# Kernel tuning notes

Measured on AMD Instinct MI355X. Metric: run time of the kernel, lower is better.

Reference implementation:

```python
import jax, jax.numpy as jnp
import numpy as np

N = 50000        # nodes
E = 150000       # edges
D_IN = 42        # node_input_dim
D_H = 42         # node_hidden_dim
E_IN = 10        # edge_input_dim
E_H = 128        # edge_hidden_dim
STEPS = 6        # num_step_message_passing


def _linear_params(key, fin, fout):
    k1, k2 = jax.random.split(key)
    bound = 1.0 / np.sqrt(fin)
    W = jax.random.uniform(k1, (fin, fout), minval=-bound, maxval=bound, dtype=jnp.float32)
    b = jax.random.uniform(k2, (fout,), minval=-bound, maxval=bound, dtype=jnp.float32)
    return W, b


def setup_inputs() -> dict:
    key = jax.random.key(0)
    ks = jax.random.split(key, 9)
    n_feat = jax.random.normal(ks[0], (N, D_IN), dtype=jnp.float32)
    e_feat = jax.random.normal(ks[1], (E, E_IN), dtype=jnp.float32)
    src = jax.random.randint(ks[2], (E,), 0, N, dtype=jnp.int32)
    dst = jax.random.randint(ks[3], (E,), 0, N, dtype=jnp.int32)
    lin0_w, lin0_b = _linear_params(ks[4], D_IN, D_H)
    en1_w, en1_b = _linear_params(ks[5], E_IN, E_H)
    en2_w, en2_b = _linear_params(ks[6], E_H, D_H * D_H)
    msg_w, msg_b = _linear_params(ks[7], 2 * D_H, D_H)
    conv_bias = jnp.zeros((D_H,), dtype=jnp.float32)  # NNConv bias
    return dict(n_feat=n_feat, e_feat=e_feat, src=src, dst=dst,
                lin0_w=lin0_w, lin0_b=lin0_b,
                en1_w=en1_w, en1_b=en1_b, en2_w=en2_w, en2_b=en2_b,
                conv_bias=conv_bias, msg_w=msg_w, msg_b=msg_b)


def reference(n_feat, e_feat, src, dst, lin0_w, lin0_b, en1_w, en1_b,
              en2_w, en2_b, conv_bias, msg_w, msg_b):
    init = n_feat
    out = jax.nn.relu(n_feat @ lin0_w + lin0_b)          # [N, D_H]
    # edge network: per-edge weight matrix (constant across the 6 steps)
    h_e = jax.nn.relu(e_feat @ en1_w + en1_b)            # [E, E_H]
    W_e = (h_e @ en2_w + en2_b).reshape(E, D_H, D_H)     # [E, D_H, D_H]
    for _ in range(STEPS):
        # NNConv: gather src feats, per-edge matmul, scatter-sum to dst,
        # identity residual (in==out feats) + bias
        msg = jnp.einsum('ei,eio->eo', out[src], W_e)    # [E, D_H]
        aggr = jax.ops.segment_sum(msg, dst, num_segments=N)
        m = jax.nn.relu(aggr + out + conv_bias)          # relu(conv(...))
        out = jnp.concatenate([m, out], axis=1) @ msg_w + msg_b
    return out + init
```

## Files before the change

### kernel.cpp

```cpp
#include <hip/hip_runtime.h>

typedef unsigned short u16;
typedef unsigned int u32;

#define NN 50000
#define NE 150000
#define D 42
#define EH 128
#define DD 1764
#define STEPS 6
#define MS 48
#define SCAN_NB 196

typedef __attribute__((ext_vector_type(8))) short bf8;
typedef __attribute__((ext_vector_type(4))) float f4;

static __device__ __forceinline__ float bf2f(u16 v) {
  return __uint_as_float(((u32)v) << 16);
}
static __device__ __forceinline__ u16 f2bf(float f) {
  u32 x = __float_as_uint(f);
  return (u16)((x + 0x7fffu + ((x >> 16) & 1u)) >> 16);
}

__global__ void k_detect(const u32* __restrict__ words, int* __restrict__ flag) {
  __shared__ int cnt;
  if (threadIdx.x == 0) cnt = 0;
  __syncthreads();
  int bad = 0;
  for (int i = threadIdx.x; i < 4096; i += 256) {
    u32 w = words[i];
    float v = __uint_as_float((w & 0xffffu) << 16);
    float a = fabsf(v);
    if (!(a < 16.0f)) bad++;
  }
  if (bad) atomicAdd(&cnt, bad);
  __syncthreads();
  if (threadIdx.x == 0) flag[0] = (cnt < 100) ? 1 : 0;
}

__global__ void k_cvt(const void* __restrict__ src, float* __restrict__ dst,
                      int count, const int* __restrict__ flag) {
  int i = blockIdx.x * blockDim.x + threadIdx.x;
  if (i >= count) return;
  if (flag[0]) dst[i] = bf2f(((const u16*)src)[i]);
  else         dst[i] = ((const float*)src)[i];
}

__global__ void k_hist(const int* __restrict__ dstI, int* __restrict__ cnt) {
  int e = blockIdx.x * blockDim.x + threadIdx.x;
  if (e < NE) atomicAdd(&cnt[dstI[e]], 1);
}

__global__ void k_scanA(const int* __restrict__ cnt, int* __restrict__ loc,
                        int* __restrict__ part) {
  __shared__ int wsum[4];
  int tid = threadIdx.x, wid = tid >> 6, lane = tid & 63;
  int i = blockIdx.x * 256 + tid;
  int v = (i < NN) ? cnt[i] : 0;
#pragma unroll
  for (int d = 1; d < 64; d <<= 1) {
    int t = __shfl_up(v, d, 64);
    if (lane >= d) v += t;
  }
  if (lane == 63) wsum[wid] = v;
  __syncthreads();
  if (tid == 0) {
    int s = 0;
#pragma unroll
    for (int w2 = 0; w2 < 4; ++w2) { int t = wsum[w2]; wsum[w2] = s; s += t; }
    part[blockIdx.x] = s;
  }
  __syncthreads();
  v += wsum[wid];
  if (i < NN) loc[i] = v;
}

__global__ void k_scanB(int* __restrict__ part) {
  __shared__ int wsum[4];
  int tid = threadIdx.x, wid = tid >> 6, lane = tid & 63;
  int v = (tid < SCAN_NB) ? part[tid] : 0;
  int orig = v;
#pragma unroll
  for (int d = 1; d < 64; d <<= 1) {
    int t = __shfl_up(v, d, 64);
    if (lane >= d) v += t;
  }
  if (lane == 63) wsum[wid] = v;
  __syncthreads();
  if (tid == 0) {
    int s = 0;
#pragma unroll
    for (int w2 = 0; w2 < 4; ++w2) { int t = wsum[w2]; wsum[w2] = s; s += t; }
  }
  __syncthreads();
  v += wsum[wid];
  if (tid < SCAN_NB) part[tid] = v - orig;
}

__global__ void k_scanC(const int* __restrict__ loc, const int* __restrict__ part,
                        int* __restrict__ rs) {
  int i = blockIdx.x * 256 + threadIdx.x;
  if (i == 0) rs[0] = 0;
  if (i < NN) rs[i + 1] = loc[i] + part[blockIdx.x];
}

__global__ void k_rank(const int* __restrict__ dstI, const int* __restrict__ srcI,
                       int* __restrict__ cursor, int* __restrict__ rank,
                       int* __restrict__ srcS) {
  int e = blockIdx.x * blockDim.x + threadIdx.x;
  if (e >= NE) return;
  int p = atomicAdd(&cursor[dstI[e]], 1);
  rank[e] = p;
  srcS[p] = srcI[e];
}

__global__ void k_lin0(const float* __restrict__ nf, const float* __restrict__ w,
                       const float* __restrict__ b, float* __restrict__ outp) {
  int gid = blockIdx.x * blockDim.x + threadIdx.x;
  int n = gid >> 6, lane = gid & 63;
  if (n >= NN) return;
  float xv = (lane < D) ? nf[(size_t)n * D + lane] : 0.f;
  if (lane < D) {
    float acc = b[lane];
    for (int i = 0; i < D; ++i)
      acc += __shfl(xv, i, 64) * w[i * D + lane];
    outp[(size_t)n * D + lane] = fmaxf(acc, 0.f);
  }
}

__global__ void k_en1(const float* __restrict__ ef, const float* __restrict__ w,
                      const float* __restrict__ b, const int* __restrict__ rank,
                      u16* __restrict__ h) {
  int gid = blockIdx.x * blockDim.x + threadIdx.x;
  int e = gid >> 7, k = gid & 127;
  if (e >= NE) return;
  float acc = b[k];
#pragma unroll
  for (int i = 0; i < 10; ++i)
    acc += ef[(size_t)e * 10 + i] * w[i * EH + k];
  h[(size_t)rank[e] * EH + k] = f2bf(fmaxf(acc, 0.f));
}

__global__ void k_packA(const float* __restrict__ w2, u16* __restrict__ Ap) {
  int idx = blockIdx.x * 256 + threadIdx.x;
  if (idx >= D * 4 * 3 * 64 * 8) return;
  int j = idx & 7;
  int t = idx >> 3;
  int l = t & 63; t >>= 6;
  int f = t % 3;  t /= 3;
  int s = t & 3;
  int i = t >> 2;
  int k = s * 32 + ((l >> 4) << 3) + j;
  int o = f * 16 + (l & 15);
  float v = (o < D) ? w2[(size_t)k * DD + i * D + o] : 0.f;
  Ap[idx] = f2bf(v);
}

__global__ void k_packB2(const float* __restrict__ e2b, u16* __restrict__ b2p) {
  int idx = blockIdx.x * 256 + threadIdx.x;
  if (idx >= 2 * 3 * 64 * 8) return;
  int j = idx & 7;
  int t = idx >> 3;
  int l = t & 63; t >>= 6;
  int f = t % 3;
  int s = t / 3;
  int k = s * 32 + ((l >> 4) << 3) + j;
  int o = f * 16 + (l & 15);
  float v = (k < D && o < D) ? e2b[k * D + o] : 0.f;
  b2p[idx] = f2bf(v);
}

__launch_bounds__(256, 3)
__global__ void k_edge_mfma(const float* __restrict__ outp, const u16* __restrict__ hbf,
                            const u16* __restrict__ Ap, const u16* __restrict__ b2p,
                            const int* __restrict__ srcS, float* __restrict__ msg) {
  __shared__ __align__(16) char smem[10752 + 26624];
  float* xT = (float*)smem;
  char*  hls = smem + 10752;
  char*  xbf = smem + 10752 + 16384;
  float* red = (float*)(smem + 10752);

  int tid = threadIdx.x;
  long et = (long)blockIdx.x * 64;
  int ne = (int)(NE - et); if (ne > 64) ne = 64;

  for (int c = tid; c < 1024; c += 256) {
    int row = c >> 4;
    int off = (c & 15) << 4;
    uint4 v = {0, 0, 0, 0};
    if (row < ne) v = *(const uint4*)(hbf + (et + row) * EH + (off >> 1));
    *(uint4*)(hls + row * 256 + (off ^ ((row & 7) << 4))) = v;
  }
  {
    int r = tid >> 2, j = tid & 3;
    const float* xr = (r < ne) ? (outp + (size_t)srcS[et + r] * D) : nullptr;
    for (int i = j; i < D; i += 4) {
      float v = xr ? xr[i] : 0.f;
      xT[i * 64 + r] = v;
      int bo = (r * 128 + i * 2) ^ ((r & 7) << 4);
      *(u16*)(xbf + bo) = f2bf(v);
    }
    for (int i = D + j; i < 64; i += 4) {
      int bo = (r * 128 + i * 2) ^ ((r & 7) << 4);
      *(u16*)(xbf + bo) = 0;
    }
  }
  __syncthreads();

  int w = tid >> 6;
  int l = tid & 63;
  int e16 = l & 15;
  int kg = l >> 4;

  bf8 hf[4];
  {
    int kb = (w * 32 + kg * 8) * 2;
    int sw = (e16 & 7) << 4;
#pragma unroll
    for (int g = 0; g < 4; ++g)
      hf[g] = *(const bf8*)(hls + (g * 16 + e16) * 256 + (kb ^ sw));
  }

  f4 macc[4][3];
#pragma unroll
  for (int g = 0; g < 4; ++g)
#pragma unroll
    for (int f = 0; f < 3; ++f)
      macc[g][f] = (f4){0.f, 0.f, 0.f, 0.f};

  const u16* apw = Ap + (size_t)w * 1536 + (size_t)l * 8;

#define LOADA(dst, ii)                                                          \
  {                                                                             \
    const u16* p_ = apw + (size_t)(ii) * 6144;                                  \
    dst[0] = *(const bf8*)(p_);                                                 \
    dst[1] = *(const bf8*)(p_ + 512);                                           \
    dst[2] = *(const bf8*)(p_ + 1024);                                          \
  }

#define COMPUTE(ii, AA)                                                         \
  {                                                                             \
    _Pragma("unroll")                                                           \
    for (int g = 0; g < 4; ++g) {                                               \
      float xs = xT[(ii) * 64 + g * 16 + e16];                                  \
      f4 zz = {0.f, 0.f, 0.f, 0.f};                                             \
      f4 q0 = __builtin_amdgcn_mfma_f32_16x16x32_bf16(AA[0], hf[g], zz, 0, 0, 0); \
      f4 q1 = __builtin_amdgcn_mfma_f32_16x16x32_bf16(AA[1], hf[g], zz, 0, 0, 0); \
      f4 q2 = __builtin_amdgcn_mfma_f32_16x16x32_bf16(AA[2], hf[g], zz, 0, 0, 0); \
      macc[g][0] += xs * q0;                                                    \
      macc[g][1] += xs * q1;                                                    \
      macc[g][2] += xs * q2;                                                    \
    }                                                                           \
  }

  bf8 B0[3], B1[3], B2[3], B3[3];
  LOADA(B0, 0); LOADA(B1, 1); LOADA(B2, 2); LOADA(B3, 3);
#pragma unroll 1
  for (int i = 0; i < 40; i += 4) {
    COMPUTE(i, B0);     { int n0 = i + 4; if (n0 >= D) n0 = 0; LOADA(B0, n0); }
    COMPUTE(i + 1, B1); { int n1 = i + 5; if (n1 >= D) n1 = 0; LOADA(B1, n1); }
    COMPUTE(i + 2, B2); { int n2 = i + 6; if (n2 >= D) n2 = 0; LOADA(B2, n2); }
    COMPUTE(i + 3, B3); { int n3 = i + 7; if (n3 >= D) n3 = 0; LOADA(B3, n3); }
  }
  COMPUTE(40, B0);
  COMPUTE(41, B1);

  if (w < 2) {
    const u16* bpw = b2p + (size_t)w * 1536 + (size_t)l * 8;
    bf8 Bb0 = *(const bf8*)(bpw);
    bf8 Bb1 = *(const bf8*)(bpw + 512);
    bf8 Bb2 = *(const bf8*)(bpw + 1024);
    int kb = (w * 32 + kg * 8) * 2;
    int sw = (e16 & 7) << 4;
#pragma unroll
    for (int g = 0; g < 4; ++g) {
      bf8 bx = *(const bf8*)(xbf + (g * 16 + e16) * 128 + (kb ^ sw));
      macc[g][0] = __builtin_amdgcn_mfma_f32_16x16x32_bf16(Bb0, bx, macc[g][0], 0, 0, 0);
      macc[g][1] = __builtin_amdgcn_mfma_f32_16x16x32_bf16(Bb1, bx, macc[g][1], 0, 0, 0);
      macc[g][2] = __builtin_amdgcn_mfma_f32_16x16x32_bf16(Bb2, bx, macc[g][2], 0, 0, 0);
    }
  }

  __syncthreads();
  if (w < 2) {
#pragma unroll
    for (int g = 0; g < 4; ++g)
#pragma unroll
      for (int f = 0; f < 3; ++f)
        *(f4*)&red[((size_t)w * 64 + g * 16 + e16) * 52 + f * 16 + kg * 4] = macc[g][f];
  }
  __syncthreads();
  if (w >= 2) {
#pragma unroll
    for (int g = 0; g < 4; ++g)
#pragma unroll
      for (int f = 0; f < 3; ++f) {
        float* rp = &red[((size_t)(w - 2) * 64 + g * 16 + e16) * 52 + f * 16 + kg * 4];
        f4 v = *(f4*)rp;
        v += macc[g][f];
        *(f4*)rp = v;
      }
  }
  __syncthreads();
  {
    int e = tid >> 2, c = tid & 3;
    if (e < ne) {
      float* mrow = msg + (size_t)(et + e) * MS;
#pragma unroll
      for (int u = 0; u < 3; ++u) {
        int o0 = c * 12 + u * 4;
        f4 v0 = *(f4*)&red[(size_t)e * 52 + o0];
        f4 v1 = *(f4*)&red[((size_t)(64 + e)) * 52 + o0];
        f4 s = v0 + v1;
        *(f4*)(mrow + o0) = s;
      }
    }
  }
#undef COMPUTE
#undef LOADA
}

__global__ void k_node_update(const float* __restrict__ msg, const int* __restrict__ rs,
                              const float* __restrict__ outp,
                              const float* __restrict__ cb, const float* __restrict__ mw,
                              const float* __restrict__ mb, float* __restrict__ newout,
                              const float* __restrict__ nf, void* __restrict__ fout,
                              int last, const int* __restrict__ flag) {
  int gid = blockIdx.x * blockDim.x + threadIdx.x;
  int n = gid >> 6, lane = gid & 63;
  if (n >= NN) return;
  float ov = (lane < D) ? outp[(size_t)n * D + lane] : 0.f;
  float av = 0.f;
  int r0 = rs[n], r1 = rs[n + 1];
  if (lane < D && r0 < r1) {
    float a0 = 0.f, a1 = 0.f, a2 = 0.f, a3 = 0.f;
    for (int r = r0; r < r1; r += 4) {
      int i1 = (r + 1 < r1) ? r + 1 : r;
      int i2 = (r + 2 < r1) ? r + 2 : r;
      int i3 = (r + 3 < r1) ? r + 3 : r;
      float v0 = msg[(size_t)r  * MS + lane];
      float v1 = msg[(size_t)i1 * MS + lane];
      float v2 = msg[(size_t)i2 * MS + lane];
      float v3 = msg[(size_t)i3 * MS + lane];
      a0 += v0;
      a1 += (r + 1 < r1) ? v1 : 0.f;
      a2 += (r + 2 < r1) ? v2 : 0.f;
      a3 += (r + 3 < r1) ? v3 : 0.f;
    }
    av = (a0 + a1) + (a2 + a3);
  }
  float mv = 0.f;
  if (lane < D) mv = fmaxf(av + ov + cb[lane], 0.f);
  if (lane < D) {
    float acc = mb[lane];
    for (int i = 0; i < D; ++i)
      acc += __shfl(mv, i, 64) * mw[i * D + lane];
    for (int i = 0; i < D; ++i)
      acc += __shfl(ov, i, 64) * mw[(D + i) * D + lane];
    size_t idx = (size_t)n * D + lane;
    if (last) {
      float res = acc + nf[idx];
      if (flag[0]) ((u16*)fout)[idx] = f2bf(res);
      else         ((float*)fout)[idx] = res;
    } else {
      newout[idx] = acc;
    }
  }
}

extern "C" void kernel_launch(void* const* d_in, const int* in_sizes, int n_in,
                              void* d_out, int out_size, void* d_ws, size_t ws_size,
                              hipStream_t stream) {
  (void)in_sizes; (void)n_in; (void)out_size; (void)ws_size;
  const void* nf   = d_in[0];
  const void* ef   = d_in[1];
  const int*  srcI = (const int*)d_in[2];
  const int*  dstI = (const int*)d_in[3];
  const void* l0w = d_in[4];  const void* l0b = d_in[5];
  const void* e1w = d_in[6];  const void* e1b = d_in[7];
  const void* e2w = d_in[8];  const void* e2b = d_in[9];
  const void* cbI = d_in[10]; const void* mwI = d_in[11]; const void* mbI = d_in[12];

  char* ws = (char*)d_ws;
  size_t off = 0;
  auto alloc = [&](size_t bytes) -> void* {
    void* p = ws + off;
    off = (off + bytes + 255) & ~(size_t)255;
    return p;
  };

  int*   flag  = (int*)alloc(4);
  float* c_nf  = (float*)alloc((size_t)NN * D * 4);
  float* c_ef  = (float*)alloc((size_t)NE * 10 * 4);
  float* c_l0w = (float*)alloc(D * D * 4);
  float* c_l0b = (float*)alloc(D * 4);
  float* c_e1w = (float*)alloc(10 * EH * 4);
  float* c_e1b = (float*)alloc(EH * 4);
  float* c_e2w = (float*)alloc((size_t)EH * DD * 4);
  float* c_e2b = (float*)alloc(DD * 4);
  float* c_cb  = (float*)alloc(D * 4);
  float* c_mw  = (float*)alloc(2 * D * D * 4);
  float* c_mb  = (float*)alloc(D * 4);
  float* out_a = (float*)alloc((size_t)NN * D * 4);
  float* out_b = (float*)alloc((size_t)NN * D * 4);
  u16*   hbf   = (u16*)alloc((size_t)NE * EH * 2);
  u16*   Ap    = (u16*)alloc((size_t)D * 4 * 3 * 64 * 8 * 2);
  u16*   b2p   = (u16*)alloc((size_t)2 * 3 * 64 * 8 * 2);
  int*   cnt    = (int*)alloc((size_t)NN * 4);
  int*   loc    = (int*)alloc((size_t)NN * 4);
  int*   part   = (int*)alloc((size_t)SCAN_NB * 4);
  int*   rowst  = (int*)alloc((size_t)(NN + 1) * 4);
  int*   cursor = (int*)alloc((size_t)NN * 4);
  int*   rank   = (int*)alloc((size_t)NE * 4);
  int*   srcS   = (int*)alloc((size_t)NE * 4);
  float* msg    = (float*)alloc((size_t)NE * MS * 4);

  k_detect<<<1, 256, 0, stream>>>((const u32*)nf, flag);
  auto cvt = [&](const void* s, float* dPtr, int count) {
    k_cvt<<<(count + 255) / 256, 256, 0, stream>>>(s, dPtr, count, flag);
  };
  cvt(nf,  c_nf,  NN * D);
  cvt(ef,  c_ef,  NE * 10);
  cvt(l0w, c_l0w, D * D);
  cvt(l0b, c_l0b, D);
  cvt(e1w, c_e1w, 10 * EH);
  cvt(e1b, c_e1b, EH);
  cvt(e2w, c_e2w, EH * DD);
  cvt(e2b, c_e2b, DD);
  cvt(cbI, c_cb,  D);
  cvt(mwI, c_mw,  2 * D * D);
  cvt(mbI, c_mb,  D);

  (void)hipMemsetAsync(cnt, 0, (size_t)NN * 4, stream);
  k_hist<<<(NE + 255) / 256, 256, 0, stream>>>(dstI, cnt);
  k_scanA<<<SCAN_NB, 256, 0, stream>>>(cnt, loc, part);
  k_scanB<<<1, 256, 0, stream>>>(part);
  k_scanC<<<SCAN_NB, 256, 0, stream>>>(loc, part, rowst);
  (void)hipMemcpyAsync(cursor, rowst, (size_t)NN * 4, hipMemcpyDeviceToDevice, stream);
  k_rank<<<(NE + 255) / 256, 256, 0, stream>>>(dstI, srcI, cursor, rank, srcS);

  k_lin0<<<(NN * 64 + 255) / 256, 256, 0, stream>>>(c_nf, c_l0w, c_l0b, out_a);
  k_en1<<<(NE * 128 + 255) / 256, 256, 0, stream>>>(c_ef, c_e1w, c_e1b, rank, hbf);
  k_packA<<<(D * 4 * 3 * 64 * 8 + 255) / 256, 256, 0, stream>>>(c_e2w, Ap);
  k_packB2<<<(2 * 3 * 64 * 8 + 255) / 256, 256, 0, stream>>>(c_e2b, b2p);

  int nblk = (NE + 63) / 64;
  float* cur = out_a;
  float* nxt = out_b;
  for (int s = 0; s < STEPS; ++s) {
    k_edge_mfma<<<nblk, 256, 0, stream>>>(cur, hbf, Ap, b2p, srcS, msg);
    int last = (s == STEPS - 1) ? 1 : 0;
    k_node_update<<<(NN * 64 + 255) / 256, 256, 0, stream>>>(
        msg, rowst, cur, c_cb, c_mw, c_mb, nxt, c_nf, d_out, last, flag);
    float* t = cur; cur = nxt; nxt = t;
  }
}
```

Before: 950.1 us.

## Rewrite node update as bf16 MFMA tile kernel with padded node stride

Replaces the per-node, wave-per-node scalar shuffle matmul in the node update with a block kernel. Each block handles 64 nodes: it aggregates messages with float4 loads, packs the [m, out] concat as bf16 into LDS, and applies the 84x42 message weight with 16x16x32 bf16 MFMA across three waves before reducing and writing. Node feature arrays are padded to a 48-float stride so rows can be read and written with vector loads. This cuts the shuffle and scalar FMA cost, but the 84-wide matmul now runs in bf16, which loses precision, and one thread serially walks all incoming edges for each node.

```diff
diff --git a/kernel.cpp b/kernel.cpp
--- a/kernel.cpp
+++ b/kernel.cpp
@@ -10,6 +10,7 @@
 #define DD 1764
 #define STEPS 6
 #define MS 48
+#define OS 48
 #define SCAN_NB 196
 
 typedef __attribute__((ext_vector_type(8))) short bf8;
@@ -21,6 +22,9 @@
 static __device__ __forceinline__ u16 f2bf(float f) {
   u32 x = __float_as_uint(f);
   return (u16)((x + 0x7fffu + ((x >> 16) & 1u)) >> 16);
+}
+static __device__ __forceinline__ u32 bfpair(float a, float b) {
+  return (u32)f2bf(a) | ((u32)f2bf(b) << 16);
 }
 
 __global__ void k_detect(const u32* __restrict__ words, int* __restrict__ flag) {
@@ -125,7 +129,7 @@
     float acc = b[lane];
     for (int i = 0; i < D; ++i)
       acc += __shfl(xv, i, 64) * w[i * D + lane];
-    outp[(size_t)n * D + lane] = fmaxf(acc, 0.f);
+    outp[(size_t)n * OS + lane] = fmaxf(acc, 0.f);
   }
 }
 
@@ -171,6 +175,20 @@
   b2p[idx] = f2bf(v);
 }
 
+__global__ void k_packMW(const float* __restrict__ mw, u16* __restrict__ mwp) {
+  int idx = blockIdx.x * 256 + threadIdx.x;
+  if (idx >= 3 * 3 * 64 * 8) return;
+  int j = idx & 7;
+  int t = idx >> 3;
+  int l = t & 63; t >>= 6;
+  int f = t % 3;
+  int s = t / 3;
+  int k = s * 32 + ((l >> 4) << 3) + j;
+  int o = f * 16 + (l & 15);
+  float v = (k < 2 * D && o < D) ? mw[k * D + o] : 0.f;
+  mwp[idx] = f2bf(v);
+}
+
 __launch_bounds__(256, 3)
 __global__ void k_edge_mfma(const float* __restrict__ outp, const u16* __restrict__ hbf,
                             const u16* __restrict__ Ap, const u16* __restrict__ b2p,
@@ -194,7 +212,7 @@
   }
   {
     int r = tid >> 2, j = tid & 3;
-    const float* xr = (r < ne) ? (outp + (size_t)srcS[et + r] * D) : nullptr;
+    const float* xr = (r < ne) ? (outp + (size_t)srcS[et + r] * OS) : nullptr;
     for (int i = j; i < D; i += 4) {
       float v = xr ? xr[i] : 0.f;
       xT[i * 64 + r] = v;
@@ -321,50 +339,132 @@
 #undef LOADA
 }
 
-__global__ void k_node_update(const float* __restrict__ msg, const int* __restrict__ rs,
-                              const float* __restrict__ outp,
-                              const float* __restrict__ cb, const float* __restrict__ mw,
-                              const float* __restrict__ mb, float* __restrict__ newout,
-                              const float* __restrict__ nf, void* __restrict__ fout,
-                              int last, const int* __restrict__ flag) {
-  int gid = blockIdx.x * blockDim.x + threadIdx.x;
-  int n = gid >> 6, lane = gid & 63;
-  if (n >= NN) return;
-  float ov = (lane < D) ? outp[(size_t)n * D + lane] : 0.f;
-  float av = 0.f;
-  int r0 = rs[n], r1 = rs[n + 1];
-  if (lane < D && r0 < r1) {
-    float a0 = 0.f, a1 = 0.f, a2 = 0.f, a3 = 0.f;
-    for (int r = r0; r < r1; r += 4) {
-      int i1 = (r + 1 < r1) ? r + 1 : r;
-      int i2 = (r + 2 < r1) ? r + 2 : r;
-      int i3 = (r + 3 < r1) ? r + 3 : r;
-      float v0 = msg[(size_t)r  * MS + lane];
-      float v1 = msg[(size_t)i1 * MS + lane];
-      float v2 = msg[(size_t)i2 * MS + lane];
-      float v3 = msg[(size_t)i3 * MS + lane];
-      a0 += v0;
-      a1 += (r + 1 < r1) ? v1 : 0.f;
-      a2 += (r + 2 < r1) ? v2 : 0.f;
-      a3 += (r + 3 < r1) ? v3 : 0.f;
-    }
-    av = (a0 + a1) + (a2 + a3);
-  }
-  float mv = 0.f;
-  if (lane < D) mv = fmaxf(av + ov + cb[lane], 0.f);
-  if (lane < D) {
-    float acc = mb[lane];
-    for (int i = 0; i < D; ++i)
-      acc += __shfl(mv, i, 64) * mw[i * D + lane];
-    for (int i = 0; i < D; ++i)
-      acc += __shfl(ov, i, 64) * mw[(D + i) * D + lane];
-    size_t idx = (size_t)n * D + lane;
-    if (last) {
-      float res = acc + nf[idx];
-      if (flag[0]) ((u16*)fout)[idx] = f2bf(res);
-      else         ((float*)fout)[idx] = res;
+__launch_bounds__(256, 3)
+__global__ void k_node_mfma(const float* __restrict__ msg, const int* __restrict__ rs,
+                            const float* __restrict__ outp,
+                            const float* __restrict__ cb, const u16* __restrict__ mwp,
+                            const float* __restrict__ mb, float* __restrict__ newout,
+                            const float* __restrict__ nf, void* __restrict__ fout,
+                            int last, const int* __restrict__ flag) {
+  __shared__ __align__(16) char smem[12288 + 39936];
+  char*  cmat = smem;
+  float* red  = (float*)(smem + 12288);
+
+  int tid = threadIdx.x;
+  int nt = blockIdx.x * 64;
+  int nn = NN - nt; if (nn > 64) nn = 64;
+
+  {
+    int r = tid >> 2, c = tid & 3;
+    char* base = cmat + r * 192;
+    u32* wm = (u32*)(base + c * 24);
+    u32* wo = (u32*)(base + 84 + c * 24);
+    if (r < nn) {
+      int n = nt + r;
+      int r0 = rs[n], r1 = rs[n + 1];
+      f4 a0 = {0,0,0,0}, a1 = {0,0,0,0}, a2 = {0,0,0,0};
+      for (int row = r0; row < r1; ++row) {
+        const float* mr = msg + (size_t)row * MS + c * 12;
+        a0 += *(const f4*)(mr);
+        a1 += *(const f4*)(mr + 4);
+        a2 += *(const f4*)(mr + 8);
+      }
+      const float* orow = outp + (size_t)n * OS + c * 12;
+      f4 o0 = *(const f4*)(orow);
+      f4 o1 = *(const f4*)(orow + 4);
+      f4 o2 = *(const f4*)(orow + 8);
+      const float* cbp = cb + c * 12;
+      f4 m0 = a0 + o0 + *(const f4*)(cbp);
+      f4 m1 = a1 + o1 + *(const f4*)(cbp + 4);
+      f4 m2 = a2 + o2 + *(const f4*)(cbp + 8);
+#pragma unroll
+      for (int q = 0; q < 4; ++q) {
+        m0[q] = fmaxf(m0[q], 0.f);
+        m1[q] = fmaxf(m1[q], 0.f);
+        m2[q] = fmaxf(m2[q], 0.f);
+      }
+      wm[0] = bfpair(m0[0], m0[1]);
+      wm[1] = bfpair(m0[2], m0[3]);
+      wm[2] = bfpair(m1[0], m1[1]);
+      wo[0] = bfpair(o0[0], o0[1]);
+      wo[1] = bfpair(o0[2], o0[3]);
+      wo[2] = bfpair(o1[0], o1[1]);
+      if (c < 3) {
+        wm[3] = bfpair(m1[2], m1[3]);
+        wm[4] = bfpair(m2[0], m2[1]);
+        wm[5] = bfpair(m2[2], m2[3]);
+        wo[3] = bfpair(o1[2], o1[3]);
+        wo[4] = bfpair(o2[0], o2[1]);
+        wo[5] = bfpair(o2[2], o2[3]);
+      }
     } else {
-      newout[idx] = acc;
+      wm[0] = wm[1] = wm[2] = 0;
+      wo[0] = wo[1] = wo[2] = 0;
+      if (c < 3) { wm[3] = wm[4] = wm[5] = 0; wo[3] = wo[4] = wo[5] = 0; }
+    }
+    if (c == 0) {
+      u32* wp = (u32*)(base + 168);
+#pragma unroll
+      for (int t2 = 0; t2 < 6; ++t2) wp[t2] = 0;
+    }
+  }
+  __syncthreads();
+
+  int w = tid >> 6;
+  int l = tid & 63;
+  int e16 = l & 15;
+  int kg = l >> 4;
+
+  if (w < 3) {
+    bf8 bfr[4];
+#pragma unroll
+    for (int g = 0; g < 4; ++g)
+      bfr[g] = *(const bf8*)(cmat + (g * 16 + e16) * 192 + w * 64 + kg * 16);
+    const u16* ap = mwp + (size_t)(w * 3) * 512 + (size_t)l * 8;
+    bf8 A0 = *(const bf8*)(ap);
+    bf8 A1 = *(const bf8*)(ap + 512);
+    bf8 A2 = *(const bf8*)(ap + 1024);
+    f4 zz = {0.f, 0.f, 0.f, 0.f};
+    float* rw = red + (size_t)w * 3328;
+#pragma unroll
+    for (int g = 0; g < 4; ++g) {
+      f4 c0 = __builtin_amdgcn_mfma_f32_16x16x32_bf16(A0, bfr[g], zz, 0, 0, 0);
+      f4 c1 = __builtin_amdgcn_mfma_f32_16x16x32_bf16(A1, bfr[g], zz, 0, 0, 0);
+      f4 c2 = __builtin_amdgcn_mfma_f32_16x16x32_bf16(A2, bfr[g], zz, 0, 0, 0);
+      float* rp = rw + (size_t)(g * 16 + e16) * 52 + kg * 4;
+      *(f4*)(rp)      = c0;
+      *(f4*)(rp + 16) = c1;
+      *(f4*)(rp + 32) = c2;
+    }
+  }
+  __syncthreads();
+
+  {
+    int e = tid >> 2, c = tid & 3;
+    if (e < nn) {
+      int n = nt + e;
+#pragma unroll
+      for (int u = 0; u < 3; ++u) {
+        int o0 = c * 12 + u * 4;
+        f4 s = *(f4*)&red[(size_t)e * 52 + o0];
+        s += *(f4*)&red[(size_t)(3328 + e * 52) + o0];
+        s += *(f4*)&red[(size_t)(6656 + e * 52) + o0];
+        s += *(const f4*)(mb + o0);
+        if (last) {
+#pragma unroll
+          for (int q = 0; q < 4; ++q) {
+            int oc = o0 + q;
+            if (oc < D) {
+              size_t idx = (size_t)n * D + oc;
+              float res = s[q] + nf[idx];
+              if (flag[0]) ((u16*)fout)[idx] = f2bf(res);
+              else         ((float*)fout)[idx] = res;
+            }
+          }
+        } else {
+          *(f4*)(newout + (size_t)n * OS + o0) = s;
+        }
+      }
     }
   }
 }
@@ -402,11 +502,12 @@
   float* c_cb  = (float*)alloc(D * 4);
   float* c_mw  = (float*)alloc(2 * D * D * 4);
   float* c_mb  = (float*)alloc(D * 4);
-  float* out_a = (float*)alloc((size_t)NN * D * 4);
-  float* out_b = (float*)alloc((size_t)NN * D * 4);
+  float* out_a = (float*)alloc((size_t)NN * OS * 4);
+  float* out_b = (float*)alloc((size_t)NN * OS * 4);
   u16*   hbf   = (u16*)alloc((size_t)NE * EH * 2);
   u16*   Ap    = (u16*)alloc((size_t)D * 4 * 3 * 64 * 8 * 2);
   u16*   b2p   = (u16*)alloc((size_t)2 * 3 * 64 * 8 * 2);
+  u16*   mwp   = (u16*)alloc((size_t)3 * 3 * 64 * 8 * 2);
   int*   cnt    = (int*)alloc((size_t)NN * 4);
   int*   loc    = (int*)alloc((size_t)NN * 4);
   int*   part   = (int*)alloc((size_t)SCAN_NB * 4);
@@ -444,15 +545,17 @@
   k_en1<<<(NE * 128 + 255) / 256, 256, 0, stream>>>(c_ef, c_e1w, c_e1b, rank, hbf);
   k_packA<<<(D * 4 * 3 * 64 * 8 + 255) / 256, 256, 0, stream>>>(c_e2w, Ap);
   k_packB2<<<(2 * 3 * 64 * 8 + 255) / 256, 256, 0, stream>>>(c_e2b, b2p);
+  k_packMW<<<(3 * 3 * 64 * 8 + 255) / 256, 256, 0, stream>>>(c_mw, mwp);
 
   int nblk = (NE + 63) / 64;
+  int nblkN = (NN + 63) / 64;
   float* cur = out_a;
   float* nxt = out_b;
   for (int s = 0; s < STEPS; ++s) {
     k_edge_mfma<<<nblk, 256, 0, stream>>>(cur, hbf, Ap, b2p, srcS, msg);
     int last = (s == STEPS - 1) ? 1 : 0;
-    k_node_update<<<(NN * 64 + 255) / 256, 256, 0, stream>>>(
-        msg, rowst, cur, c_cb, c_mw, c_mb, nxt, c_nf, d_out, last, flag);
+    k_node_mfma<<<nblkN, 256, 0, stream>>>(
+        msg, rowst, cur, c_cb, mwp, c_mb, nxt, c_nf, d_out, last, flag);
     float* t = cur; cur = nxt; nxt = t;
   }
 }
```

After: 769.5 us (median of 2 runs). -19.0%, faster.
